# Performance work log

Measured on AMD Instinct MI355X. Metric: run time of the kernel, lower is better.

## Reference

```python
import jax, jax.numpy as jnp
import numpy as np

D_IN = 768      # encoder feature dim (hardcoded in GRUCell(768, d_model))
D_MODEL = 256   # hidden size
B, T = 64, 512


def _gru_cell(x, h, W_ih, W_hh, b_ih, b_hh):
    # PyTorch GRUCell math. W_ih: [in, 3H], W_hh: [H, 3H], biases [3H].
    gi = x @ W_ih + b_ih
    gh = h @ W_hh + b_hh
    i_r, i_z, i_n = jnp.split(gi, 3, axis=-1)
    h_r, h_z, h_n = jnp.split(gh, 3, axis=-1)
    r = jax.nn.sigmoid(i_r + h_r)
    z = jax.nn.sigmoid(i_z + h_z)
    n = jnp.tanh(i_n + r * h_n)
    return (1.0 - z) * n + z * h


def setup_inputs() -> dict:
    key = jax.random.key(0)
    ks = jax.random.split(key, 10)
    s_in = 1.0 / np.sqrt(D_MODEL)
    inp = {
        "encoder_outputs": jax.random.normal(ks[0], (B, T, D_IN), jnp.float32),
        "tau1": jnp.array([1.0], jnp.float32),
        "tau2": jnp.array([1.2], jnp.float32),
        "W_ih1": jax.random.normal(ks[1], (D_IN, 3 * D_MODEL), jnp.float32) * s_in,
        "W_hh1": jax.random.normal(ks[2], (D_MODEL, 3 * D_MODEL), jnp.float32) * s_in,
        "b_ih1": jax.random.normal(ks[3], (3 * D_MODEL,), jnp.float32) * s_in,
        "b_hh1": jax.random.normal(ks[4], (3 * D_MODEL,), jnp.float32) * s_in,
        "W_ih2": jax.random.normal(ks[5], (D_IN + D_MODEL, 3 * D_MODEL), jnp.float32) * s_in,
        "W_hh2": jax.random.normal(ks[6], (D_MODEL, 3 * D_MODEL), jnp.float32) * s_in,
        "b_ih2": jax.random.normal(ks[7], (3 * D_MODEL,), jnp.float32) * s_in,
        "b_hh2": jax.random.normal(ks[8], (3 * D_MODEL,), jnp.float32) * s_in,
    }
    return inp


def reference(encoder_outputs, tau1, tau2, W_ih1, W_hh1, b_ih1, b_hh1,
              W_ih2, W_hh2, b_ih2, b_hh2):
    bsz = encoder_outputs.shape[0]
    inv_t1 = 1.0 / tau1  # [1], broadcasts over [B, H]
    inv_t2 = 1.0 / tau2
    h0 = (jnp.zeros((bsz, D_MODEL), encoder_outputs.dtype),
          jnp.zeros((bsz, D_MODEL), encoder_outputs.dtype))

    xs = jnp.swapaxes(encoder_outputs, 0, 1)  # [T, B, D_IN]

    def step(carry, x_t):
        h1, h2 = carry
        h1_ = _gru_cell(x_t, h1, W_ih1, W_hh1, b_ih1, b_hh1)
        h1 = (1.0 - inv_t1) * h1 + inv_t1 * h1_
        x2 = jnp.concatenate([x_t, h1], axis=1)
        h2_ = _gru_cell(x2, h2, W_ih2, W_hh2, b_ih2, b_hh2)
        h2 = (1.0 - inv_t2) * h2 + inv_t2 * h2_
        return (h1, h2), (h1, h2)

    _, (o1, o2) = jax.lax.scan(step, h0, xs)  # each [T, B, H]
    out = jnp.concatenate([o1, o2], axis=2)   # [T, B, 2H]
    out = jnp.swapaxes(out, 0, 1)             # [B, T, 2H]
    # Note: F.dropout(p=0.5) in the original is stochastic; omitted here
    # (identity) so the reference is deterministic for kernel comparison.
    return out
```

## Files before the change

### kernel.cpp

```cpp
#include <hip/hip_runtime.h>

typedef _Float16 f16;
typedef _Float16 f16x2 __attribute__((ext_vector_type(2)));
typedef _Float16 f16x8 __attribute__((ext_vector_type(8)));
typedef float f32x4 __attribute__((ext_vector_type(4)));
typedef unsigned int u32;
typedef unsigned short u16;

#define B_SZ 64
#define T_SZ 512
#define DIN 768
#define H_SZ 256
#define TH 768
#define M_ROWS (B_SZ * T_SZ)

#define O_WT1 ((size_t)0)
#define O_WT2 (O_WT1 + (size_t)768 * 768 * 2)
#define O_H1 (O_WT2 + (size_t)768 * 1024 * 2)
#define O_G (O_H1 + (size_t)M_ROWS * H_SZ * 2)

__device__ __forceinline__ u32 pk2(float a, float b) {
  union { f16 h[2]; u32 u; } x;
  x.h[0] = (f16)a;
  x.h[1] = (f16)b;
  return x.u;
}

__device__ __forceinline__ float dot2f(u32 w, u32 h, float acc) {
#if __has_builtin(__builtin_amdgcn_fdot2)
  union { u32 u; f16x2 v; } a, b;
  a.u = w;
  b.u = h;
  return __builtin_amdgcn_fdot2(a.v, b.v, acc, false);
#else
  union { u32 u; f16 h[2]; } a, b;
  a.u = w;
  b.u = h;
  acc = fmaf((float)a.h[0], (float)b.h[0], acc);
  acc = fmaf((float)a.h[1], (float)b.h[1], acc);
  return acc;
#endif
}

__device__ __forceinline__ float sigmf_(float x) {
  return 1.0f / (1.0f + __expf(-x));
}
__device__ __forceinline__ float tanhf_(float x) {
  float e = __expf(-2.0f * fabsf(x));
  float r = (1.0f - e) / (1.0f + e);
  return copysignf(r, x);
}

__global__ __launch_bounds__(256) void k_transpose(const float* __restrict__ W,
                                                   f16* __restrict__ Wt, int K,
                                                   int N) {
  __shared__ f16 tile[32][33];
  int tx = threadIdx.x, ty = threadIdx.y;
  int n0 = blockIdx.x * 32, k0 = blockIdx.y * 32;
#pragma unroll
  for (int q = 0; q < 4; ++q) {
    int k = k0 + ty + q * 8;
    tile[ty + q * 8][tx] = (f16)W[(size_t)k * N + n0 + tx];
  }
  __syncthreads();
#pragma unroll
  for (int q = 0; q < 4; ++q) {
    int n = n0 + ty + q * 8;
    Wt[(size_t)n * K + k0 + tx] = tile[tx][ty + q * 8];
  }
}

#define LDK 40
__global__ __launch_bounds__(256, 2) void k_gemm(
    const float* __restrict__ A32, const f16* __restrict__ AH,
    const f16* __restrict__ Bt, const float* __restrict__ bias,
    f16* __restrict__ C, int K, int bstride) {
  __shared__ __align__(16) f16 Asm[128 * LDK];
  __shared__ __align__(16) f16 Bsm[128 * LDK];
  int tid = threadIdx.x;
  int lane = tid & 63, wave = tid >> 6;
  int wm = wave & 1, wn = wave >> 1;
  int fm = lane & 15, fk = (lane >> 4) * 8;
  int srow = tid >> 1, skp = (tid & 1) * 16;
  size_t r0 = (size_t)blockIdx.y * 128;
  int n0 = blockIdx.x * 128;
  f32x4 acc[4][4] = {};

  for (int k0 = 0; k0 < K; k0 += 32) {
    __syncthreads();
    if (k0 < DIN) {
      const float* src = A32 + (r0 + srow) * DIN + k0 + skp;
      float4 v0 = *(const float4*)(src);
      float4 v1 = *(const float4*)(src + 4);
      float4 v2 = *(const float4*)(src + 8);
      float4 v3 = *(const float4*)(src + 12);
      uint4 w0 = make_uint4(pk2(v0.x, v0.y), pk2(v0.z, v0.w), pk2(v1.x, v1.y),
                            pk2(v1.z, v1.w));
      uint4 w1 = make_uint4(pk2(v2.x, v2.y), pk2(v2.z, v2.w), pk2(v3.x, v3.y),
                            pk2(v3.z, v3.w));
      *(uint4*)&Asm[srow * LDK + skp] = w0;
      *(uint4*)&Asm[srow * LDK + skp + 8] = w1;
    } else {
      const uint4* src =
          (const uint4*)(AH + (r0 + srow) * H_SZ + (k0 - DIN) + skp);
      *(uint4*)&Asm[srow * LDK + skp] = src[0];
      *(uint4*)&Asm[srow * LDK + skp + 8] = src[1];
    }
    const uint4* bsrc =
        (const uint4*)(Bt + (size_t)(n0 + srow) * bstride + k0 + skp);
    *(uint4*)&Bsm[srow * LDK + skp] = bsrc[0];
    *(uint4*)&Bsm[srow * LDK + skp + 8] = bsrc[1];
    __syncthreads();

    f16x8 af[4], bf[4];
#pragma unroll
    for (int mt = 0; mt < 4; ++mt)
      af[mt] = *(const f16x8*)&Asm[(wm * 64 + mt * 16 + fm) * LDK + fk];
#pragma unroll
    for (int nt = 0; nt < 4; ++nt)
      bf[nt] = *(const f16x8*)&Bsm[(wn * 64 + nt * 16 + fm) * LDK + fk];
#pragma unroll
    for (int mt = 0; mt < 4; ++mt)
#pragma unroll
      for (int nt = 0; nt < 4; ++nt)
        acc[mt][nt] = __builtin_amdgcn_mfma_f32_16x16x32_f16(af[mt], bf[nt],
                                                             acc[mt][nt], 0, 0, 0);
  }

  int ccol = lane & 15, crb = (lane >> 4) * 4;
#pragma unroll
  for (int nt = 0; nt < 4; ++nt) {
    int col = n0 + wn * 64 + nt * 16 + ccol;
    float bv = bias[col];
#pragma unroll
    for (int mt = 0; mt < 4; ++mt) {
      size_t rb = r0 + wm * 64 + mt * 16 + crb;
#pragma unroll
      for (int rg = 0; rg < 4; ++rg)
        C[(rb + rg) * TH + col] = (f16)(acc[mt][nt][rg] + bv);
    }
  }
}

__global__ __launch_bounds__(512, 2) void k_rec(
    const f16* __restrict__ G, const float* __restrict__ Whh,
    const float* __restrict__ bhh, const float* __restrict__ tau,
    float* __restrict__ out, int out_off, f16* __restrict__ H1out) {
  __shared__ __align__(16) u16 s_h16[256];
  __shared__ float s_h32[256];
  __shared__ float s_part[256 * 3];
  __shared__ __align__(16) f16 s_stage[32 * TH];

  int tid = threadIdx.x;
  int b = blockIdx.x;
  int cg = tid & 255;
  int kh = tid >> 8;

  u32 w2[3][64];
#pragma unroll
  for (int ch = 0; ch < 8; ++ch) {
    int kc = ch * 32;
    __syncthreads();
#pragma unroll
    for (int q = 0; q < 12; ++q) {
      int idx4 = tid + q * 512;
      float4 v = *(const float4*)(Whh + (size_t)kc * TH + (size_t)idx4 * 4);
      union { f16 h[4]; uint2 u; } pw;
      pw.h[0] = (f16)v.x;
      pw.h[1] = (f16)v.y;
      pw.h[2] = (f16)v.z;
      pw.h[3] = (f16)v.w;
      *(uint2*)&s_stage[idx4 * 4] = pw.u;
    }
    __syncthreads();
    if ((kc >> 7) == kh) {
      int ib = (kc & 127) >> 1;
#pragma unroll
      for (int i2 = 0; i2 < 16; ++i2) {
#pragma unroll
        for (int c = 0; c < 3; ++c) {
          int col = cg + c * 256;
          w2[c][ib + i2] = pk2((float)s_stage[(2 * i2) * TH + col],
                               (float)s_stage[(2 * i2 + 1) * TH + col]);
        }
      }
    }
  }

  float bb0 = bhh[cg], bb1 = bhh[cg + 256], bb2 = bhh[cg + 512];
  float invt = 1.0f / tau[0];
  float om = 1.0f - invt;
  if (tid < 256) {
    s_h16[tid] = 0;
    s_h32[tid] = 0.0f;
  }
  __syncthreads();

  const f16* gbase = G + (size_t)b * T_SZ * TH;
  float* obase = out + (size_t)b * T_SZ * 512 + out_off;
  f16* hbase = H1out ? H1out + (size_t)b * T_SZ * H_SZ : (f16*)0;
  const uint4* hv4 = (const uint4*)s_h16 + kh * 16;

  for (int t = 0; t < T_SZ; ++t) {
    f16 gg0 = (f16)0.f, gg1 = (f16)0.f, gg2 = (f16)0.f;
    if (tid < 256) {
      const f16* gp = gbase + (size_t)t * TH + cg;
      gg0 = gp[0];
      gg1 = gp[256];
      gg2 = gp[512];
    }
    float a0 = 0.f, a1 = 0.f, a2 = 0.f;
#pragma unroll
    for (int ii = 0; ii < 16; ++ii) {
      uint4 hv = hv4[ii];
      a0 = dot2f(w2[0][ii * 4 + 0], hv.x, a0);
      a1 = dot2f(w2[1][ii * 4 + 0], hv.x, a1);
      a2 = dot2f(w2[2][ii * 4 + 0], hv.x, a2);
      a0 = dot2f(w2[0][ii * 4 + 1], hv.y, a0);
      a1 = dot2f(w2[1][ii * 4 + 1], hv.y, a1);
      a2 = dot2f(w2[2][ii * 4 + 1], hv.y, a2);
      a0 = dot2f(w2[0][ii * 4 + 2], hv.z, a0);
      a1 = dot2f(w2[1][ii * 4 + 2], hv.z, a1);
      a2 = dot2f(w2[2][ii * 4 + 2], hv.z, a2);
      a0 = dot2f(w2[0][ii * 4 + 3], hv.w, a0);
      a1 = dot2f(w2[1][ii * 4 + 3], hv.w, a1);
      a2 = dot2f(w2[2][ii * 4 + 3], hv.w, a2);
    }
    if (kh) {
      s_part[cg * 3 + 0] = a0;
      s_part[cg * 3 + 1] = a1;
      s_part[cg * 3 + 2] = a2;
    }
    __syncthreads();
    if (tid < 256) {
      float ghr = a0 + s_part[cg * 3 + 0] + bb0;
      float ghz = a1 + s_part[cg * 3 + 1] + bb1;
      float ghn = a2 + s_part[cg * 3 + 2] + bb2;
      float r = sigmf_((float)gg0 + ghr);
      float z = sigmf_((float)gg1 + ghz);
      float n = tanhf_((float)gg2 + r * ghn);
      float hold = s_h32[cg];
      float hc = (1.0f - z) * n + z * hold;
      float hn2 = om * hold + invt * hc;
      s_h32[cg] = hn2;
      union { f16 h; u16 s; } hb;
      hb.h = (f16)hn2;
      s_h16[cg] = hb.s;
      obase[(size_t)t * 512 + cg] = hn2;
      if (hbase) hbase[(size_t)t * H_SZ + cg] = (f16)hn2;
    }
    __syncthreads();
  }
}

extern "C" void kernel_launch(void* const* d_in, const int* in_sizes, int n_in,
                              void* d_out, int out_size, void* d_ws,
                              size_t ws_size, hipStream_t stream) {
  const float* enc = (const float*)d_in[0];
  const float* tau1 = (const float*)d_in[1];
  const float* tau2 = (const float*)d_in[2];
  const float* Wih1 = (const float*)d_in[3];
  const float* Whh1 = (const float*)d_in[4];
  const float* bih1 = (const float*)d_in[5];
  const float* bhh1 = (const float*)d_in[6];
  const float* Wih2 = (const float*)d_in[7];
  const float* Whh2 = (const float*)d_in[8];
  const float* bih2 = (const float*)d_in[9];
  const float* bhh2 = (const float*)d_in[10];
  float* out = (float*)d_out;
  char* ws = (char*)d_ws;

  f16* Wt1 = (f16*)(ws + O_WT1);
  f16* Wt2 = (f16*)(ws + O_WT2);
  f16* H1 = (f16*)(ws + O_H1);
  f16* G = (f16*)(ws + O_G);

  k_transpose<<<dim3(24, 24), dim3(32, 8), 0, stream>>>(Wih1, Wt1, 768, 768);
  k_transpose<<<dim3(24, 32), dim3(32, 8), 0, stream>>>(Wih2, Wt2, 1024, 768);

  k_gemm<<<dim3(6, 256), 256, 0, stream>>>(enc, (const f16*)0, Wt1, bih1, G,
                                           768, 768);
  k_rec<<<64, 512, 0, stream>>>(G, Whh1, bhh1, tau1, out, 0, H1);

  k_gemm<<<dim3(6, 256), 256, 0, stream>>>(enc, H1, Wt2, bih2, G, 1024, 1024);
  k_rec<<<64, 512, 0, stream>>>(G, Whh2, bhh2, tau2, out, 256, (f16*)0);
}
```

Baseline: 1.515 ms.

## Remap recurrent GRU kernel to one thread per gate column with 768 threads

The recurrent kernel now launches 768 threads per block, each owning one gate column of W_hh across the full 256-wide hidden dimension. Weights are held in 128 named u32 registers per thread, replacing the earlier 3x64 register array split across two K halves. This drops the cross-half partial-sum reduction, and the z and n-gate partials pass to the first 256 threads through shared memory. The aim is to spread each step's dot-product work over more wavefronts to cut serial latency per timestep, at the cost of more shared staging and fewer registers available per thread under the new launch bounds.

```diff
diff --git a/kernel.cpp b/kernel.cpp
--- a/kernel.cpp
+++ b/kernel.cpp
@@ -142,52 +142,104 @@
   }
 }
 
-__global__ __launch_bounds__(512, 2) void k_rec(
+#define DECLW(c)                                                               \
+  u32 w##c##_0, w##c##_1, w##c##_2, w##c##_3, w##c##_4, w##c##_5, w##c##_6,    \
+      w##c##_7, w##c##_8, w##c##_9, w##c##_10, w##c##_11, w##c##_12,           \
+      w##c##_13, w##c##_14, w##c##_15
+
+#define STAGE_CHUNK(CH)                                                        \
+  __syncthreads();                                                             \
+  _Pragma("unroll") for (int q = 0; q < 8; ++q) {                              \
+    int idx4 = tid + q * 768;                                                  \
+    float4 v = *(const float4*)(Whh + (size_t)(CH)*32 * TH + (size_t)idx4 * 4);\
+    union { f16 h[4]; uint2 u; } pw;                                           \
+    pw.h[0] = (f16)v.x;                                                        \
+    pw.h[1] = (f16)v.y;                                                        \
+    pw.h[2] = (f16)v.z;                                                        \
+    pw.h[3] = (f16)v.w;                                                        \
+    *(uint2*)&s_stage[idx4 * 4] = pw.u;                                        \
+  }                                                                            \
+  __syncthreads();
+
+#define PKW(CH, I, R0, R1)                                                     \
+  w##CH##_##I =                                                                \
+      pk2((float)s_stage[(R0)*TH + tid], (float)s_stage[(R1)*TH + tid])
+
+#define LOADW(CH)                                                              \
+  STAGE_CHUNK(CH)                                                              \
+  PKW(CH, 0, 0, 1);                                                            \
+  PKW(CH, 1, 2, 3);                                                            \
+  PKW(CH, 2, 4, 5);                                                            \
+  PKW(CH, 3, 6, 7);                                                            \
+  PKW(CH, 4, 8, 9);                                                            \
+  PKW(CH, 5, 10, 11);                                                          \
+  PKW(CH, 6, 12, 13);                                                          \
+  PKW(CH, 7, 14, 15);                                                          \
+  PKW(CH, 8, 16, 17);                                                          \
+  PKW(CH, 9, 18, 19);                                                          \
+  PKW(CH, 10, 20, 21);                                                         \
+  PKW(CH, 11, 22, 23);                                                         \
+  PKW(CH, 12, 24, 25);                                                         \
+  PKW(CH, 13, 26, 27);                                                         \
+  PKW(CH, 14, 28, 29);                                                         \
+  PKW(CH, 15, 30, 31)
+
+#define DOTCH(CH, ACC)                                                         \
+  {                                                                            \
+    uint4 hv = hvp[4 * (CH) + 0];                                              \
+    ACC = dot2f(w##CH##_0, hv.x, ACC);                                         \
+    ACC = dot2f(w##CH##_1, hv.y, ACC);                                         \
+    ACC = dot2f(w##CH##_2, hv.z, ACC);                                         \
+    ACC = dot2f(w##CH##_3, hv.w, ACC);                                         \
+    hv = hvp[4 * (CH) + 1];                                                    \
+    ACC = dot2f(w##CH##_4, hv.x, ACC);                                         \
+    ACC = dot2f(w##CH##_5, hv.y, ACC);                                         \
+    ACC = dot2f(w##CH##_6, hv.z, ACC);                                         \
+    ACC = dot2f(w##CH##_7, hv.w, ACC);                                         \
+    hv = hvp[4 * (CH) + 2];                                                    \
+    ACC = dot2f(w##CH##_8, hv.x, ACC);                                         \
+    ACC = dot2f(w##CH##_9, hv.y, ACC);                                         \
+    ACC = dot2f(w##CH##_10, hv.z, ACC);                                        \
+    ACC = dot2f(w##CH##_11, hv.w, ACC);                                        \
+    hv = hvp[4 * (CH) + 3];                                                    \
+    ACC = dot2f(w##CH##_12, hv.x, ACC);                                        \
+    ACC = dot2f(w##CH##_13, hv.y, ACC);                                        \
+    ACC = dot2f(w##CH##_14, hv.z, ACC);                                        \
+    ACC = dot2f(w##CH##_15, hv.w, ACC);                                        \
+  }
+
+__global__ __launch_bounds__(768, 3) void k_rec(
     const f16* __restrict__ G, const float* __restrict__ Whh,
     const float* __restrict__ bhh, const float* __restrict__ tau,
     float* __restrict__ out, int out_off, f16* __restrict__ H1out) {
   __shared__ __align__(16) u16 s_h16[256];
   __shared__ float s_h32[256];
-  __shared__ float s_part[256 * 3];
-  __shared__ __align__(16) f16 s_stage[32 * TH];
+  __shared__ float s_pz[256];
+  __shared__ float s_pnh[256];
+  __shared__ float s_pni[256];
+  __shared__ __align__(16) f16 s_stage[56 * TH];
 
   int tid = threadIdx.x;
   int b = blockIdx.x;
-  int cg = tid & 255;
-  int kh = tid >> 8;
-
-  u32 w2[3][64];
-#pragma unroll
-  for (int ch = 0; ch < 8; ++ch) {
-    int kc = ch * 32;
-    __syncthreads();
-#pragma unroll
-    for (int q = 0; q < 12; ++q) {
-      int idx4 = tid + q * 512;
-      float4 v = *(const float4*)(Whh + (size_t)kc * TH + (size_t)idx4 * 4);
-      union { f16 h[4]; uint2 u; } pw;
-      pw.h[0] = (f16)v.x;
-      pw.h[1] = (f16)v.y;
-      pw.h[2] = (f16)v.z;
-      pw.h[3] = (f16)v.w;
-      *(uint2*)&s_stage[idx4 * 4] = pw.u;
-    }
-    __syncthreads();
-    if ((kc >> 7) == kh) {
-      int ib = (kc & 127) >> 1;
-#pragma unroll
-      for (int i2 = 0; i2 < 16; ++i2) {
-#pragma unroll
-        for (int c = 0; c < 3; ++c) {
-          int col = cg + c * 256;
-          w2[c][ib + i2] = pk2((float)s_stage[(2 * i2) * TH + col],
-                               (float)s_stage[(2 * i2 + 1) * TH + col]);
-        }
-      }
-    }
-  }
-
-  float bb0 = bhh[cg], bb1 = bhh[cg + 256], bb2 = bhh[cg + 512];
+
+  DECLW(0);
+  DECLW(1);
+  DECLW(2);
+  DECLW(3);
+  DECLW(4);
+  DECLW(5);
+  DECLW(6);
+  DECLW(7);
+  LOADW(0);
+  LOADW(1);
+  LOADW(2);
+  LOADW(3);
+  LOADW(4);
+  LOADW(5);
+  LOADW(6);
+  LOADW(7);
+
+  float bb = bhh[tid];
   float invt = 1.0f / tau[0];
   float om = 1.0f - invt;
   if (tid < 256) {
@@ -199,55 +251,40 @@
   const f16* gbase = G + (size_t)b * T_SZ * TH;
   float* obase = out + (size_t)b * T_SZ * 512 + out_off;
   f16* hbase = H1out ? H1out + (size_t)b * T_SZ * H_SZ : (f16*)0;
-  const uint4* hv4 = (const uint4*)s_h16 + kh * 16;
+  const uint4* hvp = (const uint4*)s_h16;
 
   for (int t = 0; t < T_SZ; ++t) {
-    f16 gg0 = (f16)0.f, gg1 = (f16)0.f, gg2 = (f16)0.f;
-    if (tid < 256) {
-      const f16* gp = gbase + (size_t)t * TH + cg;
-      gg0 = gp[0];
-      gg1 = gp[256];
-      gg2 = gp[512];
-    }
-    float a0 = 0.f, a1 = 0.f, a2 = 0.f;
-#pragma unroll
-    for (int ii = 0; ii < 16; ++ii) {
-      uint4 hv = hv4[ii];
-      a0 = dot2f(w2[0][ii * 4 + 0], hv.x, a0);
-      a1 = dot2f(w2[1][ii * 4 + 0], hv.x, a1);
-      a2 = dot2f(w2[2][ii * 4 + 0], hv.x, a2);
-      a0 = dot2f(w2[0][ii * 4 + 1], hv.y, a0);
-      a1 = dot2f(w2[1][ii * 4 + 1], hv.y, a1);
-      a2 = dot2f(w2[2][ii * 4 + 1], hv.y, a2);
-      a0 = dot2f(w2[0][ii * 4 + 2], hv.z, a0);
-      a1 = dot2f(w2[1][ii * 4 + 2], hv.z, a1);
-      a2 = dot2f(w2[2][ii * 4 + 2], hv.z, a2);
-      a0 = dot2f(w2[0][ii * 4 + 3], hv.w, a0);
-      a1 = dot2f(w2[1][ii * 4 + 3], hv.w, a1);
-      a2 = dot2f(w2[2][ii * 4 + 3], hv.w, a2);
-    }
-    if (kh) {
-      s_part[cg * 3 + 0] = a0;
-      s_part[cg * 3 + 1] = a1;
-      s_part[cg * 3 + 2] = a2;
+    float gg = (float)gbase[(size_t)t * TH + tid];
+    float aA = 0.f, aB = 0.f;
+    DOTCH(0, aA);
+    DOTCH(1, aB);
+    DOTCH(2, aA);
+    DOTCH(3, aB);
+    DOTCH(4, aA);
+    DOTCH(5, aB);
+    DOTCH(6, aA);
+    DOTCH(7, aB);
+    float a = aA + aB + bb;
+    if (tid >= 512) {
+      s_pnh[tid - 512] = a;
+      s_pni[tid - 512] = gg;
+    } else if (tid >= 256) {
+      s_pz[tid - 256] = a + gg;
     }
     __syncthreads();
     if (tid < 256) {
-      float ghr = a0 + s_part[cg * 3 + 0] + bb0;
-      float ghz = a1 + s_part[cg * 3 + 1] + bb1;
-      float ghn = a2 + s_part[cg * 3 + 2] + bb2;
-      float r = sigmf_((float)gg0 + ghr);
-      float z = sigmf_((float)gg1 + ghz);
-      float n = tanhf_((float)gg2 + r * ghn);
-      float hold = s_h32[cg];
+      float r = sigmf_(a + gg);
+      float z = sigmf_(s_pz[tid]);
+      float n = tanhf_(s_pni[tid] + r * s_pnh[tid]);
+      float hold = s_h32[tid];
       float hc = (1.0f - z) * n + z * hold;
       float hn2 = om * hold + invt * hc;
-      s_h32[cg] = hn2;
+      s_h32[tid] = hn2;
       union { f16 h; u16 s; } hb;
       hb.h = (f16)hn2;
-      s_h16[cg] = hb.s;
-      obase[(size_t)t * 512 + cg] = hn2;
-      if (hbase) hbase[(size_t)t * H_SZ + cg] = (f16)hn2;
+      s_h16[tid] = hb.s;
+      obase[(size_t)t * 512 + tid] = hn2;
+      if (hbase) hbase[(size_t)t * H_SZ + tid] = (f16)hn2;
     }
     __syncthreads();
   }
@@ -280,8 +317,8 @@
 
   k_gemm<<<dim3(6, 256), 256, 0, stream>>>(enc, (const f16*)0, Wt1, bih1, G,
                                            768, 768);
-  k_rec<<<64, 512, 0, stream>>>(G, Whh1, bhh1, tau1, out, 0, H1);
+  k_rec<<<64, 768, 0, stream>>>(G, Whh1, bhh1, tau1, out, 0, H1);
 
   k_gemm<<<dim3(6, 256), 256, 0, stream>>>(enc, H1, Wt2, bih2, G, 1024, 1024);
-  k_rec<<<64, 512, 0, stream>>>(G, Whh2, bhh2, tau2, out, 256, (f16*)0);
-}
+  k_rec<<<64, 768, 0, stream>>>(G, Whh2, bhh2, tau2, out, 256, (f16*)0);
+}
```

Result: slower. 1.898 ms (+25.3%).

## Batch 16 sequences per block in recurrence using MFMA with register-resident W_hh

Applied to the files above, without the earlier changes.

The recurrent kernel now runs each block on 16 batch rows at once instead of one. The per-step h·W_hh product becomes 16x16x32 f16 MFMA ops, with W_hh fragments held in registers and h double-buffered in shared memory, so one barrier per step replaces two. The grid drops from 64 blocks to 4. This keeps MFMA units busy and amortises the weights across batch rows, but only 4 CUs are used, so per-step latency and the serial gate math set the cost.

```diff
diff --git a/kernel.cpp b/kernel.cpp
--- a/kernel.cpp
+++ b/kernel.cpp
@@ -24,22 +24,6 @@
   x.h[0] = (f16)a;
   x.h[1] = (f16)b;
   return x.u;
-}
-
-__device__ __forceinline__ float dot2f(u32 w, u32 h, float acc) {
-#if __has_builtin(__builtin_amdgcn_fdot2)
-  union { u32 u; f16x2 v; } a, b;
-  a.u = w;
-  b.u = h;
-  return __builtin_amdgcn_fdot2(a.v, b.v, acc, false);
-#else
-  union { u32 u; f16 h[2]; } a, b;
-  a.u = w;
-  b.u = h;
-  acc = fmaf((float)a.h[0], (float)b.h[0], acc);
-  acc = fmaf((float)a.h[1], (float)b.h[1], acc);
-  return acc;
-#endif
 }
 
 __device__ __forceinline__ float sigmf_(float x) {
@@ -142,113 +126,156 @@
   }
 }
 
-__global__ __launch_bounds__(512, 2) void k_rec(
+#define WST 48
+#define HST 280
+#define HBUF (16 * HST)
+
+__device__ __forceinline__ void stage_chunk(const float* __restrict__ Whh,
+                                            f16* __restrict__ s_wstage, int c,
+                                            int tid) {
+#pragma unroll
+  for (int qq = 0; qq < 12; ++qq) {
+    int idx4 = tid + qq * 512;
+    int kk = idx4 / 192;
+    int n4 = (idx4 - kk * 192) * 4;
+    const float* sp = Whh + ((size_t)c * 32 + kk) * TH + n4;
+    float4 v = *(const float4*)sp;
+    s_wstage[(n4 + 0) * WST + kk] = (f16)v.x;
+    s_wstage[(n4 + 1) * WST + kk] = (f16)v.y;
+    s_wstage[(n4 + 2) * WST + kk] = (f16)v.z;
+    s_wstage[(n4 + 3) * WST + kk] = (f16)v.w;
+  }
+}
+
+#define DECLBF(g, s)                                                           \
+  f16x8 bf##g##_##s##_0, bf##g##_##s##_1, bf##g##_##s##_2, bf##g##_##s##_3,    \
+      bf##g##_##s##_4, bf##g##_##s##_5, bf##g##_##s##_6, bf##g##_##s##_7
+
+#define LDF1(g, s, q)                                                          \
+  bf##g##_##s##_##q =                                                          \
+      *(const f16x8*)&s_wstage[(size_t)(256 * (g) + cwb + 16 * (s)) * WST +    \
+                               kup8]
+
+#define LDFRAGS(q)                                                             \
+  LDF1(0, 0, q);                                                               \
+  LDF1(0, 1, q);                                                               \
+  LDF1(1, 0, q);                                                               \
+  LDF1(1, 1, q);                                                               \
+  LDF1(2, 0, q);                                                               \
+  LDF1(2, 1, q)
+
+#define STAGE_AND_FRAGS(q)                                                     \
+  __syncthreads();                                                             \
+  stage_chunk(Whh, s_wstage, q, tid);                                          \
+  __syncthreads();                                                             \
+  LDFRAGS(q)
+
+#define MFMA16(d, a, b)                                                        \
+  d = __builtin_amdgcn_mfma_f32_16x16x32_f16(a, b, d, 0, 0, 0)
+
+#define MM6(AF, q)                                                             \
+  MFMA16(accr0, AF, bf0_0_##q);                                                \
+  MFMA16(accr1, AF, bf0_1_##q);                                                \
+  MFMA16(accz0, AF, bf1_0_##q);                                                \
+  MFMA16(accz1, AF, bf1_1_##q);                                                \
+  MFMA16(accn0, AF, bf2_0_##q);                                                \
+  MFMA16(accn1, AF, bf2_1_##q)
+
+#define AFLD(i, q)                                                             \
+  af##i = *(const f16x8*)&s_h[curb + l15 * HST + (q)*32 + kup8]
+
+#define DGI(s, rg) f16 gir##s##rg, giz##s##rg, gin##s##rg
+#define LDGI(s, rg)                                                            \
+  {                                                                            \
+    const f16* gp =                                                            \
+        G + ((size_t)gbase_row + (rg)*T_SZ) * TH + cwb + 16 * (s);             \
+    gir##s##rg = gp[0];                                                        \
+    giz##s##rg = gp[256];                                                      \
+    gin##s##rg = gp[512];                                                      \
+  }
+
+#define GATE(s, rg, ACCR, ACCZ, ACCN, HOLD)                                    \
+  {                                                                            \
+    float rr = sigmf_((float)gir##s##rg + ACCR[rg] + bbr##s);                  \
+    float zz = sigmf_((float)giz##s##rg + ACCZ[rg] + bbz##s);                  \
+    float nn = tanhf_((float)gin##s##rg + rr * (ACCN[rg] + bbn##s));           \
+    float ho = HOLD[rg];                                                       \
+    float hn = om * ho + invt * ((1.0f - zz) * nn + zz * ho);                  \
+    HOLD[rg] = hn;                                                             \
+    s_h[nxtb + (mm + rg) * HST + cwb + 16 * (s)] = (f16)hn;                    \
+    out_g[((size_t)gbase_row + (rg)*T_SZ) * 512 + out_off + cwb + 16 * (s)] =  \
+        hn;                                                                    \
+    if (H1out)                                                                 \
+      H1out[((size_t)gbase_row + (rg)*T_SZ) * 256 + cwb + 16 * (s)] =          \
+          (f16)hn;                                                             \
+  }
+
+__global__ __launch_bounds__(512, 1) void k_rec(
     const f16* __restrict__ G, const float* __restrict__ Whh,
     const float* __restrict__ bhh, const float* __restrict__ tau,
-    float* __restrict__ out, int out_off, f16* __restrict__ H1out) {
-  __shared__ __align__(16) u16 s_h16[256];
-  __shared__ float s_h32[256];
-  __shared__ float s_part[256 * 3];
-  __shared__ __align__(16) f16 s_stage[32 * TH];
+    float* __restrict__ out_g, int out_off, f16* __restrict__ H1out) {
+  __shared__ __align__(16) f16 s_wstage[768 * WST];
+  __shared__ __align__(16) f16 s_h[2 * HBUF];
 
   int tid = threadIdx.x;
-  int b = blockIdx.x;
-  int cg = tid & 255;
-  int kh = tid >> 8;
-
-  u32 w2[3][64];
-#pragma unroll
-  for (int ch = 0; ch < 8; ++ch) {
-    int kc = ch * 32;
-    __syncthreads();
-#pragma unroll
-    for (int q = 0; q < 12; ++q) {
-      int idx4 = tid + q * 512;
-      float4 v = *(const float4*)(Whh + (size_t)kc * TH + (size_t)idx4 * 4);
-      union { f16 h[4]; uint2 u; } pw;
-      pw.h[0] = (f16)v.x;
-      pw.h[1] = (f16)v.y;
-      pw.h[2] = (f16)v.z;
-      pw.h[3] = (f16)v.w;
-      *(uint2*)&s_stage[idx4 * 4] = pw.u;
-    }
-    __syncthreads();
-    if ((kc >> 7) == kh) {
-      int ib = (kc & 127) >> 1;
-#pragma unroll
-      for (int i2 = 0; i2 < 16; ++i2) {
-#pragma unroll
-        for (int c = 0; c < 3; ++c) {
-          int col = cg + c * 256;
-          w2[c][ib + i2] = pk2((float)s_stage[(2 * i2) * TH + col],
-                               (float)s_stage[(2 * i2 + 1) * TH + col]);
-        }
-      }
-    }
-  }
-
-  float bb0 = bhh[cg], bb1 = bhh[cg + 256], bb2 = bhh[cg + 512];
+  int lane = tid & 63;
+  int w = tid >> 6;
+  int l15 = lane & 15;
+  int kup = lane >> 4;
+  int kup8 = kup * 8;
+  int mm = kup * 4;
+  int cwb = 32 * w + l15;
+  int b0 = blockIdx.x * 16;
+
+  for (int i = tid; i < 2 * HBUF; i += 512) s_h[i] = (f16)0.f;
+
+  DECLBF(0, 0); DECLBF(0, 1); DECLBF(1, 0);
+  DECLBF(1, 1); DECLBF(2, 0); DECLBF(2, 1);
+  STAGE_AND_FRAGS(0);
+  STAGE_AND_FRAGS(1);
+  STAGE_AND_FRAGS(2);
+  STAGE_AND_FRAGS(3);
+  STAGE_AND_FRAGS(4);
+  STAGE_AND_FRAGS(5);
+  STAGE_AND_FRAGS(6);
+  STAGE_AND_FRAGS(7);
+
+  float bbr0 = bhh[cwb], bbr1 = bhh[cwb + 16];
+  float bbz0 = bhh[256 + cwb], bbz1 = bhh[256 + cwb + 16];
+  float bbn0 = bhh[512 + cwb], bbn1 = bhh[512 + cwb + 16];
   float invt = 1.0f / tau[0];
   float om = 1.0f - invt;
-  if (tid < 256) {
-    s_h16[tid] = 0;
-    s_h32[tid] = 0.0f;
-  }
+  f32x4 hold0 = {}, hold1 = {};
   __syncthreads();
 
-  const f16* gbase = G + (size_t)b * T_SZ * TH;
-  float* obase = out + (size_t)b * T_SZ * 512 + out_off;
-  f16* hbase = H1out ? H1out + (size_t)b * T_SZ * H_SZ : (f16*)0;
-  const uint4* hv4 = (const uint4*)s_h16 + kh * 16;
-
   for (int t = 0; t < T_SZ; ++t) {
-    f16 gg0 = (f16)0.f, gg1 = (f16)0.f, gg2 = (f16)0.f;
-    if (tid < 256) {
-      const f16* gp = gbase + (size_t)t * TH + cg;
-      gg0 = gp[0];
-      gg1 = gp[256];
-      gg2 = gp[512];
-    }
-    float a0 = 0.f, a1 = 0.f, a2 = 0.f;
-#pragma unroll
-    for (int ii = 0; ii < 16; ++ii) {
-      uint4 hv = hv4[ii];
-      a0 = dot2f(w2[0][ii * 4 + 0], hv.x, a0);
-      a1 = dot2f(w2[1][ii * 4 + 0], hv.x, a1);
-      a2 = dot2f(w2[2][ii * 4 + 0], hv.x, a2);
-      a0 = dot2f(w2[0][ii * 4 + 1], hv.y, a0);
-      a1 = dot2f(w2[1][ii * 4 + 1], hv.y, a1);
-      a2 = dot2f(w2[2][ii * 4 + 1], hv.y, a2);
-      a0 = dot2f(w2[0][ii * 4 + 2], hv.z, a0);
-      a1 = dot2f(w2[1][ii * 4 + 2], hv.z, a1);
-      a2 = dot2f(w2[2][ii * 4 + 2], hv.z, a2);
-      a0 = dot2f(w2[0][ii * 4 + 3], hv.w, a0);
-      a1 = dot2f(w2[1][ii * 4 + 3], hv.w, a1);
-      a2 = dot2f(w2[2][ii * 4 + 3], hv.w, a2);
-    }
-    if (kh) {
-      s_part[cg * 3 + 0] = a0;
-      s_part[cg * 3 + 1] = a1;
-      s_part[cg * 3 + 2] = a2;
-    }
-    __syncthreads();
-    if (tid < 256) {
-      float ghr = a0 + s_part[cg * 3 + 0] + bb0;
-      float ghz = a1 + s_part[cg * 3 + 1] + bb1;
-      float ghn = a2 + s_part[cg * 3 + 2] + bb2;
-      float r = sigmf_((float)gg0 + ghr);
-      float z = sigmf_((float)gg1 + ghz);
-      float n = tanhf_((float)gg2 + r * ghn);
-      float hold = s_h32[cg];
-      float hc = (1.0f - z) * n + z * hold;
-      float hn2 = om * hold + invt * hc;
-      s_h32[cg] = hn2;
-      union { f16 h; u16 s; } hb;
-      hb.h = (f16)hn2;
-      s_h16[cg] = hb.s;
-      obase[(size_t)t * 512 + cg] = hn2;
-      if (hbase) hbase[(size_t)t * H_SZ + cg] = (f16)hn2;
-    }
+    int cur = t & 1;
+    int curb = cur * HBUF, nxtb = HBUF - curb;
+    size_t gbase_row = (size_t)(b0 + mm) * T_SZ + t;
+
+    DGI(0, 0); DGI(0, 1); DGI(0, 2); DGI(0, 3);
+    LDGI(0, 0); LDGI(0, 1); LDGI(0, 2); LDGI(0, 3);
+
+    f32x4 accr0 = {}, accr1 = {}, accz0 = {}, accz1 = {}, accn0 = {},
+          accn1 = {};
+    f16x8 af0, af1, af2, af3;
+    AFLD(0, 0); AFLD(1, 1); AFLD(2, 2); AFLD(3, 3);
+    MM6(af0, 0); MM6(af1, 1); MM6(af2, 2); MM6(af3, 3);
+
+    DGI(1, 0); DGI(1, 1); DGI(1, 2); DGI(1, 3);
+    LDGI(1, 0); LDGI(1, 1); LDGI(1, 2); LDGI(1, 3);
+
+    AFLD(0, 4); AFLD(1, 5); AFLD(2, 6); AFLD(3, 7);
+    MM6(af0, 4); MM6(af1, 5); MM6(af2, 6); MM6(af3, 7);
+
+    GATE(0, 0, accr0, accz0, accn0, hold0);
+    GATE(0, 1, accr0, accz0, accn0, hold0);
+    GATE(0, 2, accr0, accz0, accn0, hold0);
+    GATE(0, 3, accr0, accz0, accn0, hold0);
+    GATE(1, 0, accr1, accz1, accn1, hold1);
+    GATE(1, 1, accr1, accz1, accn1, hold1);
+    GATE(1, 2, accr1, accz1, accn1, hold1);
+    GATE(1, 3, accr1, accz1, accn1, hold1);
     __syncthreads();
   }
 }
@@ -280,8 +307,8 @@
 
   k_gemm<<<dim3(6, 256), 256, 0, stream>>>(enc, (const f16*)0, Wt1, bih1, G,
                                            768, 768);
-  k_rec<<<64, 512, 0, stream>>>(G, Whh1, bhh1, tau1, out, 0, H1);
+  k_rec<<<4, 512, 0, stream>>>(G, Whh1, bhh1, tau1, out, 0, H1);
 
   k_gemm<<<dim3(6, 256), 256, 0, stream>>>(enc, H1, Wt2, bih2, G, 1024, 1024);
-  k_rec<<<64, 512, 0, stream>>>(G, Whh2, bhh2, tau2, out, 256, (f16*)0);
-}
+  k_rec<<<4, 512, 0, stream>>>(G, Whh2, bhh2, tau2, out, 256, (f16*)0);
+}
```

Result: slower. 5.013 ms (+231.0%).

## Stream pre-packed recurrent weights from L2 each step instead of holding them in registers

Applied to the files above, without the earlier changes.

Adds a prep kernel that packs W_hh into an fp16-pair, thread-contiguous layout in workspace, reusing the area of the W_ih transposes once each GEMM has consumed them. The recurrent kernel no longer keeps 192 weight registers per thread. Instead it re-reads the weights from global memory (L2) every timestep, using a 4-slot software pipeline of uint4 loads interleaved with the dot products. This frees registers and drops the shared-memory staging, but adds about 768KB of L2 traffic per block per step on the serial critical path.

```diff
diff --git a/kernel.cpp b/kernel.cpp
--- a/kernel.cpp
+++ b/kernel.cpp
@@ -142,50 +142,92 @@
   }
 }
 
-__global__ __launch_bounds__(512, 2) void k_rec(
-    const f16* __restrict__ G, const float* __restrict__ Whh,
+__global__ __launch_bounds__(512) void k_prepw(const float* __restrict__ Whh,
+                                               u32* __restrict__ Wp) {
+  int gid = blockIdx.x * 512 + threadIdx.x;
+  int cc = gid / 1536;
+  int r = gid - cc * 1536;
+  int c = r >> 9;
+  int t2 = r & 511;
+  int kh = t2 >> 8, cg = t2 & 255;
+  int col = cg + c * 256;
+  int kbase = kh * 128 + cc * 16;
+  u32 o0 = pk2(Whh[(size_t)(kbase + 0) * TH + col],
+               Whh[(size_t)(kbase + 1) * TH + col]);
+  u32 o1 = pk2(Whh[(size_t)(kbase + 2) * TH + col],
+               Whh[(size_t)(kbase + 3) * TH + col]);
+  u32 o2 = pk2(Whh[(size_t)(kbase + 4) * TH + col],
+               Whh[(size_t)(kbase + 5) * TH + col]);
+  u32 o3 = pk2(Whh[(size_t)(kbase + 6) * TH + col],
+               Whh[(size_t)(kbase + 7) * TH + col]);
+  u32 o4 = pk2(Whh[(size_t)(kbase + 8) * TH + col],
+               Whh[(size_t)(kbase + 9) * TH + col]);
+  u32 o5 = pk2(Whh[(size_t)(kbase + 10) * TH + col],
+               Whh[(size_t)(kbase + 11) * TH + col]);
+  u32 o6 = pk2(Whh[(size_t)(kbase + 12) * TH + col],
+               Whh[(size_t)(kbase + 13) * TH + col]);
+  u32 o7 = pk2(Whh[(size_t)(kbase + 14) * TH + col],
+               Whh[(size_t)(kbase + 15) * TH + col]);
+  *(uint4*)&Wp[(size_t)gid * 8] = make_uint4(o0, o1, o2, o3);
+  *(uint4*)&Wp[(size_t)gid * 8 + 4] = make_uint4(o4, o5, o6, o7);
+}
+
+#define WSLOT(s)                                                               \
+  uint4 sl##s##c0a, sl##s##c0b, sl##s##c1a, sl##s##c1b, sl##s##c2a, sl##s##c2b
+
+#define ISSUE(s, ch)                                                           \
+  sl##s##c0a = wp4[((ch)*3 + 0) * 1024 + tid2 + 0];                            \
+  sl##s##c0b = wp4[((ch)*3 + 0) * 1024 + tid2 + 1];                            \
+  sl##s##c1a = wp4[((ch)*3 + 1) * 1024 + tid2 + 0];                            \
+  sl##s##c1b = wp4[((ch)*3 + 1) * 1024 + tid2 + 1];                            \
+  sl##s##c2a = wp4[((ch)*3 + 2) * 1024 + tid2 + 0];                            \
+  sl##s##c2b = wp4[((ch)*3 + 2) * 1024 + tid2 + 1]
+
+#define DOTS(s, ch)                                                            \
+  {                                                                            \
+    uint4 hA = hv4[2 * (ch)], hB = hv4[2 * (ch) + 1];                          \
+    a0 = dot2f(sl##s##c0a.x, hA.x, a0);                                        \
+    a1 = dot2f(sl##s##c1a.x, hA.x, a1);                                        \
+    a2 = dot2f(sl##s##c2a.x, hA.x, a2);                                        \
+    a0 = dot2f(sl##s##c0a.y, hA.y, a0);                                        \
+    a1 = dot2f(sl##s##c1a.y, hA.y, a1);                                        \
+    a2 = dot2f(sl##s##c2a.y, hA.y, a2);                                        \
+    a0 = dot2f(sl##s##c0a.z, hA.z, a0);                                        \
+    a1 = dot2f(sl##s##c1a.z, hA.z, a1);                                        \
+    a2 = dot2f(sl##s##c2a.z, hA.z, a2);                                        \
+    a0 = dot2f(sl##s##c0a.w, hA.w, a0);                                        \
+    a1 = dot2f(sl##s##c1a.w, hA.w, a1);                                        \
+    a2 = dot2f(sl##s##c2a.w, hA.w, a2);                                        \
+    a0 = dot2f(sl##s##c0b.x, hB.x, a0);                                        \
+    a1 = dot2f(sl##s##c1b.x, hB.x, a1);                                        \
+    a2 = dot2f(sl##s##c2b.x, hB.x, a2);                                        \
+    a0 = dot2f(sl##s##c0b.y, hB.y, a0);                                        \
+    a1 = dot2f(sl##s##c1b.y, hB.y, a1);                                        \
+    a2 = dot2f(sl##s##c2b.y, hB.y, a2);                                        \
+    a0 = dot2f(sl##s##c0b.z, hB.z, a0);                                        \
+    a1 = dot2f(sl##s##c1b.z, hB.z, a1);                                        \
+    a2 = dot2f(sl##s##c2b.z, hB.z, a2);                                        \
+    a0 = dot2f(sl##s##c0b.w, hB.w, a0);                                        \
+    a1 = dot2f(sl##s##c1b.w, hB.w, a1);                                        \
+    a2 = dot2f(sl##s##c2b.w, hB.w, a2);                                        \
+  }
+
+__global__ __launch_bounds__(512)
+__attribute__((amdgpu_waves_per_eu(2, 2))) void k_rec(
+    const f16* __restrict__ G, const u32* __restrict__ Wp,
     const float* __restrict__ bhh, const float* __restrict__ tau,
     float* __restrict__ out, int out_off, f16* __restrict__ H1out) {
   __shared__ __align__(16) u16 s_h16[256];
   __shared__ float s_h32[256];
   __shared__ float s_part[256 * 3];
-  __shared__ __align__(16) f16 s_stage[32 * TH];
 
   int tid = threadIdx.x;
   int b = blockIdx.x;
   int cg = tid & 255;
   int kh = tid >> 8;
-
-  u32 w2[3][64];
-#pragma unroll
-  for (int ch = 0; ch < 8; ++ch) {
-    int kc = ch * 32;
-    __syncthreads();
-#pragma unroll
-    for (int q = 0; q < 12; ++q) {
-      int idx4 = tid + q * 512;
-      float4 v = *(const float4*)(Whh + (size_t)kc * TH + (size_t)idx4 * 4);
-      union { f16 h[4]; uint2 u; } pw;
-      pw.h[0] = (f16)v.x;
-      pw.h[1] = (f16)v.y;
-      pw.h[2] = (f16)v.z;
-      pw.h[3] = (f16)v.w;
-      *(uint2*)&s_stage[idx4 * 4] = pw.u;
-    }
-    __syncthreads();
-    if ((kc >> 7) == kh) {
-      int ib = (kc & 127) >> 1;
-#pragma unroll
-      for (int i2 = 0; i2 < 16; ++i2) {
-#pragma unroll
-        for (int c = 0; c < 3; ++c) {
-          int col = cg + c * 256;
-          w2[c][ib + i2] = pk2((float)s_stage[(2 * i2) * TH + col],
-                               (float)s_stage[(2 * i2 + 1) * TH + col]);
-        }
-      }
-    }
-  }
+  int tid2 = tid * 2;
+
+  const uint4* wp4 = (const uint4*)Wp;
 
   float bb0 = bhh[cg], bb1 = bhh[cg + 256], bb2 = bhh[cg + 512];
   float invt = 1.0f / tau[0];
@@ -200,6 +242,14 @@
   float* obase = out + (size_t)b * T_SZ * 512 + out_off;
   f16* hbase = H1out ? H1out + (size_t)b * T_SZ * H_SZ : (f16*)0;
   const uint4* hv4 = (const uint4*)s_h16 + kh * 16;
+
+  WSLOT(0);
+  WSLOT(1);
+  WSLOT(2);
+  WSLOT(3);
+  ISSUE(0, 0);
+  ISSUE(1, 1);
+  ISSUE(2, 2);
 
   for (int t = 0; t < T_SZ; ++t) {
     f16 gg0 = (f16)0.f, gg1 = (f16)0.f, gg2 = (f16)0.f;
@@ -210,22 +260,23 @@
       gg2 = gp[512];
     }
     float a0 = 0.f, a1 = 0.f, a2 = 0.f;
-#pragma unroll
-    for (int ii = 0; ii < 16; ++ii) {
-      uint4 hv = hv4[ii];
-      a0 = dot2f(w2[0][ii * 4 + 0], hv.x, a0);
-      a1 = dot2f(w2[1][ii * 4 + 0], hv.x, a1);
-      a2 = dot2f(w2[2][ii * 4 + 0], hv.x, a2);
-      a0 = dot2f(w2[0][ii * 4 + 1], hv.y, a0);
-      a1 = dot2f(w2[1][ii * 4 + 1], hv.y, a1);
-      a2 = dot2f(w2[2][ii * 4 + 1], hv.y, a2);
-      a0 = dot2f(w2[0][ii * 4 + 2], hv.z, a0);
-      a1 = dot2f(w2[1][ii * 4 + 2], hv.z, a1);
-      a2 = dot2f(w2[2][ii * 4 + 2], hv.z, a2);
-      a0 = dot2f(w2[0][ii * 4 + 3], hv.w, a0);
-      a1 = dot2f(w2[1][ii * 4 + 3], hv.w, a1);
-      a2 = dot2f(w2[2][ii * 4 + 3], hv.w, a2);
-    }
+    ISSUE(3, 3);
+    DOTS(0, 0);
+    ISSUE(0, 4);
+    DOTS(1, 1);
+    ISSUE(1, 5);
+    DOTS(2, 2);
+    ISSUE(2, 6);
+    DOTS(3, 3);
+    ISSUE(3, 7);
+    DOTS(0, 4);
+    ISSUE(0, 0);
+    DOTS(1, 5);
+    ISSUE(1, 1);
+    DOTS(2, 6);
+    ISSUE(2, 2);
+    DOTS(3, 7);
+
     if (kh) {
       s_part[cg * 3 + 0] = a0;
       s_part[cg * 3 + 1] = a1;
@@ -274,14 +325,18 @@
   f16* Wt2 = (f16*)(ws + O_WT2);
   f16* H1 = (f16*)(ws + O_H1);
   f16* G = (f16*)(ws + O_G);
+  u32* Wp1 = (u32*)(ws + O_WT1);
+  u32* Wp2 = (u32*)(ws + O_WT2);
 
   k_transpose<<<dim3(24, 24), dim3(32, 8), 0, stream>>>(Wih1, Wt1, 768, 768);
   k_transpose<<<dim3(24, 32), dim3(32, 8), 0, stream>>>(Wih2, Wt2, 1024, 768);
 
   k_gemm<<<dim3(6, 256), 256, 0, stream>>>(enc, (const f16*)0, Wt1, bih1, G,
                                            768, 768);
-  k_rec<<<64, 512, 0, stream>>>(G, Whh1, bhh1, tau1, out, 0, H1);
+  k_prepw<<<24, 512, 0, stream>>>(Whh1, Wp1);
+  k_rec<<<64, 512, 0, stream>>>(G, Wp1, bhh1, tau1, out, 0, H1);
 
   k_gemm<<<dim3(6, 256), 256, 0, stream>>>(enc, H1, Wt2, bih2, G, 1024, 1024);
-  k_rec<<<64, 512, 0, stream>>>(G, Whh2, bhh2, tau2, out, 256, (f16*)0);
-}
+  k_prepw<<<24, 512, 0, stream>>>(Whh2, Wp2);
+  k_rec<<<64, 512, 0, stream>>>(G, Wp2, bhh2, tau2, out, 256, (f16*)0);
+}
```

New measurement: 1.539 ms. No clear change (+1.6%).
